# Performance work log

Hardware: AMD Instinct MI355X
Metric: run time of the kernel (lower is better)

Reference implementation:

```python
import jax, jax.numpy as jnp
import numpy as np

DT = 1.0
V_LAMBDA = 1e-4
V_RIDGE = 1e-4


def third_order_D(Np):
    # [Np-3, Np] banded third-difference operator
    M = Np - 3
    r = jnp.arange(M)
    D = jnp.zeros((M, Np), dtype=jnp.float32)
    D = D.at[r, r].set(-1.0).at[r, r + 1].set(3.0).at[r, r + 2].set(-3.0).at[r, r + 3].set(1.0)
    return D


def setup_inputs() -> dict:
    key = jax.random.key(0)
    k1, k2, k3 = jax.random.split(key, 3)
    B, N = 8192, 64
    dxy = jax.random.normal(k1, (B, N, 2), dtype=jnp.float32)
    theta = jax.random.normal(k2, (B, N + 1), dtype=jnp.float32)
    v0 = jax.random.normal(k3, (B,), dtype=jnp.float32)
    return {"dxy": dxy, "theta": theta, "v0": v0}


def reference(dxy, theta, v0):
    B, N, _ = dxy.shape  # theta: [B, N+1]
    g = (2.0 / DT) * dxy                     # [B, N, 2]
    b = g.reshape(B, 2 * N)                  # interleaved (x, y) per step
    cos_t = jnp.cos(theta)
    sin_t = jnp.sin(theta)

    # Assemble banded data matrix A: [B, 2N, N+1]
    rows = jnp.arange(N)
    A = jnp.zeros((B, 2 * N, N + 1), dtype=dxy.dtype)
    A = A.at[:, 2 * rows, rows].set(cos_t[:, :-1])
    A = A.at[:, 2 * rows, rows + 1].set(cos_t[:, 1:])
    A = A.at[:, 2 * rows + 1, rows].set(sin_t[:, :-1])
    A = A.at[:, 2 * rows + 1, rows + 1].set(sin_t[:, 1:])
    # data weights w = 1 -> Aw == A

    ATA = jnp.einsum('bij,bik->bjk', A, A)           # [B, N+1, N+1]
    rhs = jnp.einsum('bij,bi->bj', A[:, :, 1:], b)   # [B, N]
    rhs = rhs - ATA[:, 1:, 0] * v0[:, None]

    # Smoothness prior: third-order difference, lam3 = v_lambda / dt^6
    D3 = third_order_D(N + 1)
    DTD = (V_LAMBDA / DT ** 6) * (D3.T @ D3)         # [N+1, N+1], shared across batch
    rhs = rhs - DTD[1:, 0] * v0[:, None]

    lhs = ATA[:, 1:, 1:] + DTD[1:, 1:] + V_RIDGE * jnp.eye(N, dtype=dxy.dtype)
    L = jnp.linalg.cholesky(lhs)
    y = jax.scipy.linalg.cho_solve((L, True), rhs[..., None])[..., 0]  # [B, N]
    return jnp.concatenate([v0[:, None], y], axis=-1)                  # [B, N+1]
```

## Files before the change

### kernel.cpp

```cpp
#include <hip/hip_runtime.h>
#include <math.h>

#define LAM3  1e-4f
#define RIDGE 1e-4f
#define NN    64
#define NP    65
#define ROWS  32

__device__ __forceinline__ float d3_diag(int f) {
    if (f == 0 || f == 64) return 1.f;
    if (f == 1 || f == 63) return 10.f;
    if (f == 2 || f == 62) return 19.f;
    return 20.f;
}
__device__ __forceinline__ float d3_off1(int f) {
    if (f == 1 || f == 64) return -3.f;
    if (f == 2 || f == 63) return -12.f;
    return -15.f;
}
__device__ __forceinline__ float d3_off2(int f) {
    if (f == 2 || f == 64) return 3.f;
    return 6.f;
}

__global__ __launch_bounds__(64, 1) void alpamayo_banded_solve(
    const float* __restrict__ dxy,
    const float* __restrict__ theta,
    const float* __restrict__ v0,
    float* __restrict__ out,
    int B)
{
    __shared__ float  th_s[NP * ROWS];
    __shared__ float  dx_s[128 * ROWS];
    __shared__ float2 L12s[NN * ROWS];
    __shared__ float  rds [NN * ROWS];
    __shared__ float  outs[NP * ROWS];
    __shared__ float4 Atab[NN];

    const int lane = threadIdx.x;
    long base = (long)blockIdx.x * ROWS;
    bool fastB = true;
    if (base + ROWS > B) {
        base = B - ROWS;
        if (base < 0) { base = 0; fastB = false; }
    }

    if (lane < NN) {
        const int f = lane + 1;
        const float a0  = (f == NN ? 1.f : 2.f) + LAM3 * d3_diag(f) + RIDGE;
        const float a1c = LAM3 * d3_off1(f);
        const float a2  = LAM3 * d3_off2(f);
        float cv = 0.f;
        if (lane == 0) cv = -3.f * LAM3;
        if (lane == 1) cv =  3.f * LAM3;
        if (lane == 2) cv = -1.f * LAM3;
        Atab[lane] = make_float4(a0, a1c, a2, cv);
    }

    if (fastB) {
        const int lo = lane & 31, hi = lane >> 5;
        const float* tg = theta + (base + lo) * NP + hi;
        #pragma unroll
        for (int w = 0; w < 32; ++w) th_s[w * 64 + lane] = tg[2 * w];
        if (lane < 32) th_s[NN * 32 + lane] = theta[(base + lane) * NP + NN];
        const float* dg_ = dxy + (base + lo) * (2 * NN) + hi;
        #pragma unroll
        for (int w = 0; w < 64; ++w) dx_s[w * 64 + lane] = dg_[2 * w];
    } else {
        if (lane < B) {
            for (int f = 0; f < NP; ++f)  th_s[f * 32 + lane] = theta[((long)lane) * NP + f];
            for (int c = 0; c < 128; ++c) dx_s[c * 32 + lane] = dxy[((long)lane) * (2 * NN) + c];
        }
    }
    long v0i = base + (lane & 31); if (v0i > (long)B - 1) v0i = B - 1;
    const float v0b = v0[v0i];

    __syncthreads();

    if (lane < ROWS) {
        const int l = lane;
        float cp, sp;
        __sincosf(th_s[0 * 32 + l], &sp, &cp);
        float xc = dx_s[0 * 32 + l], yc = dx_s[1 * 32 + l];
        float thn = th_s[1 * 32 + l];
        float xn  = dx_s[2 * 32 + l], yn = dx_s[3 * 32 + l];

        float p1L1 = 0.f, p1L2 = 0.f, p2L1 = 0.f;
        float rd1 = 0.f, rd2 = 0.f, rd3 = 0.f;
        float z1 = 0.f, z2 = 0.f, z3 = 0.f;
        float* oz = outs + l * NP;
        oz[0] = v0b;

        #pragma unroll 4
        for (int i = 0; i < NN; ++i) {
            const int f = i + 1;
            const float thf = thn;
            const float xf = xn, yf = yn;
            const int f2 = (f < NN) ? f + 1 : NN;
            thn = th_s[f2 * 32 + l];
            const int c2 = (f < NN - 1) ? 2 * f + 2 : 126;
            xn = dx_s[c2 * 32 + l];
            yn = dx_s[(c2 + 1) * 32 + l];

            float cf, sf;
            __sincosf(thf, &sf, &cf);
            const float e  = cf * cp + sf * sp;
            const float xs = (f < NN) ? xf : 0.f;
            const float ys = (f < NN) ? yf : 0.f;
            const float4 a = Atab[i];
            float rr = 2.f * (cf * (xc + xs) + sf * (yc + ys));
            rr -= a.w * v0b;
            if (i == 0) rr -= e * v0b;

            const float a1  = e + a.y;
            const float Li3 = (-LAM3) * rd3;
            const float Li2 = (a.z - Li3 * p2L1) * rd2;
            const float Li1 = (a1 - Li3 * p1L2 - Li2 * p1L1) * rd1;
            const float dg  = a.x - Li3 * Li3 - Li2 * Li2 - Li1 * Li1;
            const float rd0 = __builtin_amdgcn_rsqf(dg);
            const float zi  = (rr - Li3 * z3 - Li2 * z2 - Li1 * z1) * rd0;

            L12s[i * 32 + l] = make_float2(Li1, Li2);
            rds [i * 32 + l] = rd0;
            oz[1 + i] = zi;

            p2L1 = p1L1; p1L1 = Li1; p1L2 = Li2;
            rd3 = rd2; rd2 = rd1; rd1 = rd0;
            z3 = z2; z2 = z1; z1 = zi;
            cp = cf; sp = sf; xc = xs; yc = ys;
        }

        float r1L1 = 0.f, r1L2 = 0.f, r1L3 = 0.f;
        float r2L2 = 0.f, r2L3 = 0.f, r3L3 = 0.f;
        float y1 = 0.f, y2 = 0.f, y3 = 0.f;

        float2 Lc  = L12s[(NN - 1) * 32 + l];
        float  rdc = rds [(NN - 1) * 32 + l];
        float  zc  = oz[NN];
        float  rm3 = rds [(NN - 4) * 32 + l];

        #pragma unroll 4
        for (int i = NN - 1; i >= 0; --i) {
            const float L1i = Lc.x, L2i = Lc.y, rdi = rdc, zi = zc, rdm3 = rm3;
            const int ip  = (i > 0)  ? i - 1 : 0;
            Lc  = L12s[ip * 32 + l];
            rdc = rds [ip * 32 + l];
            zc  = oz[ip + 1];
            const int im4 = (i >= 4) ? i - 4 : 0;
            rm3 = rds[im4 * 32 + l];

            const float L3i = (i >= 3) ? (-LAM3) * rdm3 : 0.f;
            const float yi  = (zi - r1L1 * y1 - r2L2 * y2 - r3L3 * y3) * rdi;
            oz[1 + i] = yi;

            r3L3 = r2L3; r2L3 = r1L3; r2L2 = r1L2;
            r1L1 = L1i;  r1L2 = L2i;  r1L3 = L3i;
            y3 = y2; y2 = y1; y1 = yi;
        }
    }

    __syncthreads();

    {
        long nv = B - base; if (nv > ROWS) nv = ROWS;
        const int nvalid = (int)nv * NP;
        float* og = out + base * NP;
        #pragma unroll
        for (int w = 0; w < 33; ++w) {
            const int q = w * 64 + lane;
            if (q < nvalid) og[q] = outs[q];
        }
    }
}

extern "C" void kernel_launch(void* const* d_in, const int* in_sizes, int n_in,
                              void* d_out, int out_size, void* d_ws, size_t ws_size,
                              hipStream_t stream) {
    const float* dxy   = (const float*)d_in[0];
    const float* theta = (const float*)d_in[1];
    const float* v0    = (const float*)d_in[2];
    float* out = (float*)d_out;
    const int B = in_sizes[2];
    const int blocks = (B + ROWS - 1) / ROWS;
    alpamayo_banded_solve<<<blocks, 64, 0, stream>>>(dxy, theta, v0, out, B);
}
```

Baseline: 75.02 us.

## Use row-major padded LDS staging with coalesced loads and direct global stores

Input staging now copies theta and dxy into shared memory with contiguous coalesced global reads, stored row-major per batch row, with dxy padded to 130 floats to avoid bank conflicts. The solve reads each row through per-lane pointers. Back-substitution results go straight to global memory, removing the output staging buffer, the final barrier and the cooperative store loop. Per-lane output stores are strided by 65 floats, so writes are uncoalesced, and row-major LDS reads may cause bank conflicts on theta.

```diff
diff --git a/kernel.cpp b/kernel.cpp
--- a/kernel.cpp
+++ b/kernel.cpp
@@ -30,11 +30,11 @@
     float* __restrict__ out,
     int B)
 {
-    __shared__ float  th_s[NP * ROWS];
-    __shared__ float  dx_s[128 * ROWS];
-    __shared__ float2 L12s[NN * ROWS];
+    __shared__ float  th_s[ROWS * NP];
+    __shared__ float  dx_s[ROWS * 130];
+    __shared__ float2 Ls2 [NN * ROWS];
     __shared__ float  rds [NN * ROWS];
-    __shared__ float  outs[NP * ROWS];
+    __shared__ float  zs  [NN * ROWS];
     __shared__ float4 Atab[NN];
 
     const int lane = threadIdx.x;
@@ -44,8 +44,9 @@
         base = B - ROWS;
         if (base < 0) { base = 0; fastB = false; }
     }
+    const int rowsValid = (B - base < ROWS) ? (int)(B - base) : ROWS;
 
-    if (lane < NN) {
+    {
         const int f = lane + 1;
         const float a0  = (f == NN ? 1.f : 2.f) + LAM3 * d3_diag(f) + RIDGE;
         const float a1c = LAM3 * d3_off1(f);
@@ -58,18 +59,21 @@
     }
 
     if (fastB) {
-        const int lo = lane & 31, hi = lane >> 5;
-        const float* tg = theta + (base + lo) * NP + hi;
+        const float* thg = theta + base * NP;
         #pragma unroll
-        for (int w = 0; w < 32; ++w) th_s[w * 64 + lane] = tg[2 * w];
-        if (lane < 32) th_s[NN * 32 + lane] = theta[(base + lane) * NP + NN];
-        const float* dg_ = dxy + (base + lo) * (2 * NN) + hi;
+        for (int w = 0; w < 32; ++w) th_s[w * 64 + lane] = thg[w * 64 + lane];
+        if (lane < 32) th_s[2048 + lane] = thg[2048 + lane];
+
+        const float* dg = dxy + base * (2 * NN);
         #pragma unroll
-        for (int w = 0; w < 64; ++w) dx_s[w * 64 + lane] = dg_[2 * w];
+        for (int w = 0; w < 64; ++w) {
+            const int q = w * 64 + lane;
+            dx_s[q + 2 * (q >> 7)] = dg[q];
+        }
     } else {
         if (lane < B) {
-            for (int f = 0; f < NP; ++f)  th_s[f * 32 + lane] = theta[((long)lane) * NP + f];
-            for (int c = 0; c < 128; ++c) dx_s[c * 32 + lane] = dxy[((long)lane) * (2 * NN) + c];
+            for (int f = 0; f < NP; ++f)  th_s[lane * NP + f]  = theta[(long)lane * NP + f];
+            for (int c = 0; c < 2 * NN; ++c) dx_s[lane * 130 + c] = dxy[(long)lane * (2 * NN) + c];
         }
     }
     long v0i = base + (lane & 31); if (v0i > (long)B - 1) v0i = B - 1;
@@ -78,36 +82,40 @@
     __syncthreads();
 
     if (lane < ROWS) {
-        const int l = lane;
+        const int  l    = lane;
+        const bool live = (l < rowsValid);
+        const float* thp = th_s + l * NP;
+        const float* dxp = dx_s + l * 130;
+        float* og = out + (base + l) * NP;
+
         float cp, sp;
-        __sincosf(th_s[0 * 32 + l], &sp, &cp);
-        float xc = dx_s[0 * 32 + l], yc = dx_s[1 * 32 + l];
-        float thn = th_s[1 * 32 + l];
-        float xn  = dx_s[2 * 32 + l], yn = dx_s[3 * 32 + l];
+        __sincosf(thp[0], &sp, &cp);
+        float xc = dxp[0], yc = dxp[1];
+        float thn = thp[1];
+        float xn = dxp[2], yn = dxp[3];
+        float4 an = Atab[0];
 
         float p1L1 = 0.f, p1L2 = 0.f, p2L1 = 0.f;
         float rd1 = 0.f, rd2 = 0.f, rd3 = 0.f;
         float z1 = 0.f, z2 = 0.f, z3 = 0.f;
-        float* oz = outs + l * NP;
-        oz[0] = v0b;
 
         #pragma unroll 4
         for (int i = 0; i < NN; ++i) {
             const int f = i + 1;
             const float thf = thn;
             const float xf = xn, yf = yn;
+            const float4 a = an;
             const int f2 = (f < NN) ? f + 1 : NN;
-            thn = th_s[f2 * 32 + l];
+            thn = thp[f2];
             const int c2 = (f < NN - 1) ? 2 * f + 2 : 126;
-            xn = dx_s[c2 * 32 + l];
-            yn = dx_s[(c2 + 1) * 32 + l];
+            xn = dxp[c2]; yn = dxp[c2 + 1];
+            an = Atab[(i < NN - 1) ? i + 1 : NN - 1];
 
             float cf, sf;
             __sincosf(thf, &sf, &cf);
             const float e  = cf * cp + sf * sp;
             const float xs = (f < NN) ? xf : 0.f;
             const float ys = (f < NN) ? yf : 0.f;
-            const float4 a = Atab[i];
             float rr = 2.f * (cf * (xc + xs) + sf * (yc + ys));
             rr -= a.w * v0b;
             if (i == 0) rr -= e * v0b;
@@ -120,9 +128,9 @@
             const float rd0 = __builtin_amdgcn_rsqf(dg);
             const float zi  = (rr - Li3 * z3 - Li2 * z2 - Li1 * z1) * rd0;
 
-            L12s[i * 32 + l] = make_float2(Li1, Li2);
-            rds [i * 32 + l] = rd0;
-            oz[1 + i] = zi;
+            Ls2[i * ROWS + l] = make_float2(Li1, Li2);
+            rds[i * ROWS + l] = rd0;
+            zs [i * ROWS + l] = zi;
 
             p2L1 = p1L1; p1L1 = Li1; p1L2 = Li2;
             rd3 = rd2; rd2 = rd1; rd1 = rd0;
@@ -130,45 +138,34 @@
             cp = cf; sp = sf; xc = xs; yc = ys;
         }
 
+        if (live) og[0] = v0b;
+
         float r1L1 = 0.f, r1L2 = 0.f, r1L3 = 0.f;
         float r2L2 = 0.f, r2L3 = 0.f, r3L3 = 0.f;
         float y1 = 0.f, y2 = 0.f, y3 = 0.f;
 
-        float2 Lc  = L12s[(NN - 1) * 32 + l];
-        float  rdc = rds [(NN - 1) * 32 + l];
-        float  zc  = oz[NN];
-        float  rm3 = rds [(NN - 4) * 32 + l];
+        float2 Lc  = Ls2[(NN - 1) * ROWS + l];
+        float  rdc = rds[(NN - 1) * ROWS + l];
+        float  zc  = zs [(NN - 1) * ROWS + l];
+        float  rm3 = rds[(NN - 4) * ROWS + l];
 
         #pragma unroll 4
         for (int i = NN - 1; i >= 0; --i) {
             const float L1i = Lc.x, L2i = Lc.y, rdi = rdc, zi = zc, rdm3 = rm3;
-            const int ip  = (i > 0)  ? i - 1 : 0;
-            Lc  = L12s[ip * 32 + l];
-            rdc = rds [ip * 32 + l];
-            zc  = oz[ip + 1];
+            const int ip = (i > 0) ? i - 1 : 0;
+            Lc  = Ls2[ip * ROWS + l];
+            rdc = rds[ip * ROWS + l];
+            zc  = zs [ip * ROWS + l];
             const int im4 = (i >= 4) ? i - 4 : 0;
-            rm3 = rds[im4 * 32 + l];
+            rm3 = rds[im4 * ROWS + l];
 
             const float L3i = (i >= 3) ? (-LAM3) * rdm3 : 0.f;
             const float yi  = (zi - r1L1 * y1 - r2L2 * y2 - r3L3 * y3) * rdi;
-            oz[1 + i] = yi;
+            if (live) og[1 + i] = yi;
 
             r3L3 = r2L3; r2L3 = r1L3; r2L2 = r1L2;
             r1L1 = L1i;  r1L2 = L2i;  r1L3 = L3i;
             y3 = y2; y2 = y1; y1 = yi;
-        }
-    }
-
-    __syncthreads();
-
-    {
-        long nv = B - base; if (nv > ROWS) nv = ROWS;
-        const int nvalid = (int)nv * NP;
-        float* og = out + base * NP;
-        #pragma unroll
-        for (int w = 0; w < 33; ++w) {
-            const int q = w * 64 + lane;
-            if (q < nvalid) og[q] = outs[q];
         }
     }
 }
```

New measurement: 73.15 us. 1.03x faster.
